# Kernel optimization log

Measured on AMD Instinct MI355X. Metric: run time of the kernel, lower is better.

Reference implementation:

```python
import jax, jax.numpy as jnp
import numpy as np

N_NODES = 100000
N_EDGES = 1600000
D_IN, D_H, D_OUT = 512, 128, 64
BN_EPS = 1e-5


def setup_inputs() -> dict:
    key = jax.random.key(0)
    ks = jax.random.split(key, 8)
    x = jax.random.normal(ks[0], (N_NODES, D_IN), dtype=jnp.float32)
    # COO sparse normalized adjacency
    row = jnp.sort(jax.random.randint(ks[1], (N_EDGES,), 0, N_NODES))
    col = jax.random.randint(ks[2], (N_EDGES,), 0, N_NODES)
    adj_vals = jax.random.uniform(ks[3], (N_EDGES,), dtype=jnp.float32) / 16.0
    # GraphConvolution params (xavier_uniform weight, zero bias)
    lim0 = float(np.sqrt(6.0 / (D_IN + D_H)))
    lim1 = float(np.sqrt(6.0 / (D_H + D_OUT)))
    W0 = jax.random.uniform(ks[4], (D_IN, D_H), minval=-lim0, maxval=lim0, dtype=jnp.float32)
    W1 = jax.random.uniform(ks[5], (D_H, D_OUT), minval=-lim1, maxval=lim1, dtype=jnp.float32)
    b0 = jnp.zeros((D_H,), dtype=jnp.float32)
    b1 = jnp.zeros((D_OUT,), dtype=jnp.float32)
    return {"x": x, "W0": W0, "b0": b0, "W1": W1, "b1": b1,
            "adj_vals": adj_vals, "row": row, "col": col}


def _spmm(vals, row, col, h, n):
    # (sparse adj) @ h : gather source rows, scale by edge value, scatter-add to dest
    return jax.ops.segment_sum(vals[:, None] * h[col], row, num_segments=n)


def reference(x, W0, b0, W1, b1, adj_vals, row, col):
    n = x.shape[0]
    # layer 0: adj @ (x @ W0) + b0  (dropout is identity in eval mode)
    h = _spmm(adj_vals, row, col, x @ W0, n) + b0
    h = jax.nn.relu(h)
    # BatchNorm1d(affine=False, track_running_stats=False): batch stats, biased var
    mean = jnp.mean(h, axis=0)
    var = jnp.mean(jnp.square(h - mean), axis=0)
    h = (h - mean) * jax.lax.rsqrt(var + BN_EPS)
    # layer 1: adj @ (h @ W1) + b1
    return _spmm(adj_vals, row, col, h @ W1, n) + b1
```

## Files before the change

kernel.cpp:

```cpp
#include <hip/hip_runtime.h>
#include <cstdint>
#include <cstddef>

#define D_IN  512
#define D_H   128
#define D_OUT 64

typedef __attribute__((ext_vector_type(8))) short bf16x8;
typedef __attribute__((ext_vector_type(4))) float f32x4;

__device__ __forceinline__ float bf2f(unsigned short u) {
  union { unsigned int i; float f; } v; v.i = ((unsigned int)u) << 16; return v.f;
}
__device__ __forceinline__ unsigned short f2bf(float f) {
  union { unsigned int i; float f; } v; v.f = f;
  unsigned int r = v.i + 0x7FFFu + ((v.i >> 16) & 1u);
  return (unsigned short)(r >> 16);
}

#define OFF_RP    0u
#define OFF_W0T   400384u
#define OFF_W1TP  531456u
#define OFF_SACC  547840u
#define OFF_CVEC  549888u
#define OFF_H     550912u
#define END_H     26150912u
#define END_HW    38950912u

__global__ void k_init(const int* __restrict__ row, int* __restrict__ rp,
                       const float* __restrict__ W0, unsigned short* __restrict__ W0t,
                       float* __restrict__ sacc, int n, int e, int RB, int TB) {
  int b = blockIdx.x, t = threadIdx.x;
  if (b < RB) {
    int i = b * 256 + t;
    if (i > n) return;
    int lo = 0, hi = e;
    while (lo < hi) { int mid = (lo + hi) >> 1; if (row[mid] < i) lo = mid + 1; else hi = mid; }
    rp[i] = lo;
  } else if (b < RB + TB) {
    int idx = (b - RB) * 256 + t;
    int k = idx & (D_IN - 1);
    int nn = idx >> 9;
    W0t[nn * D_IN + k] = f2bf(W0[k * D_H + nn]);
  } else {
    sacc[t] = 0.f;
  }
}

__global__ __launch_bounds__(256) void k_gemm1(const float* __restrict__ A,
                                               const unsigned short* __restrict__ Bt,
                                               unsigned short* __restrict__ C,
                                               int M) {
  __shared__ unsigned short Ash[2][4 * 128 * 8];
  __shared__ unsigned short Bsh[2][4 * 128 * 8];
  const int tid  = threadIdx.x;
  const int lane = tid & 63;
  const int wave = tid >> 6;
  const int wm = (wave >> 1) * 64;
  const int wn = (wave & 1) * 64;
  const int m0 = blockIdx.x * 128;
  const int quad = lane >> 4;
  const int l16  = lane & 15;
  f32x4 acc[4][4] = {};

  int am[2], ak[2];
  const float* aptr[2];
  const unsigned short* bptr[2];
#pragma unroll
  for (int i = 0; i < 2; ++i) {
    int c = tid + i * 256;
    am[i] = c >> 2; ak[i] = c & 3;
    int gm = m0 + am[i]; if (gm >= M) gm = M - 1;
    aptr[i] = A  + (size_t)gm * D_IN + ak[i] * 8;
    bptr[i] = Bt + (size_t)am[i] * D_IN + ak[i] * 8;
  }

  f32x4 areg[2][2];
  bf16x8 breg[2];
#pragma unroll
  for (int i = 0; i < 2; ++i) {
    areg[i][0] = *(const f32x4*)(aptr[i]);
    areg[i][1] = *(const f32x4*)(aptr[i] + 4);
    breg[i]    = *(const bf16x8*)(bptr[i]);
  }

  const int NIT = D_IN / 32;
  for (int it = 0; it < NIT; ++it) {
    const int buf = it & 1;
    unsigned short* ash = Ash[buf];
    unsigned short* bsh = Bsh[buf];
#pragma unroll
    for (int i = 0; i < 2; ++i) {
      bf16x8 pk;
#pragma unroll
      for (int j = 0; j < 4; ++j) {
        pk[j]     = (short)f2bf(areg[i][0][j]);
        pk[4 + j] = (short)f2bf(areg[i][1][j]);
      }
      *(bf16x8*)&ash[(ak[i] * 128 + am[i]) * 8] = pk;
      *(bf16x8*)&bsh[(ak[i] * 128 + am[i]) * 8] = breg[i];
    }
    __syncthreads();
    if (it + 1 < NIT) {
      int k0 = (it + 1) * 32;
#pragma unroll
      for (int i = 0; i < 2; ++i) {
        areg[i][0] = *(const f32x4*)(aptr[i] + k0);
        areg[i][1] = *(const f32x4*)(aptr[i] + k0 + 4);
        breg[i]    = *(const bf16x8*)(bptr[i] + k0);
      }
    }
    bf16x8 af[4], bfv[4];
#pragma unroll
    for (int mf = 0; mf < 4; ++mf)
      af[mf] = *(const bf16x8*)&ash[(quad * 128 + (wm + mf * 16 + l16)) * 8];
#pragma unroll
    for (int nf = 0; nf < 4; ++nf)
      bfv[nf] = *(const bf16x8*)&bsh[(quad * 128 + (wn + nf * 16 + l16)) * 8];
#pragma unroll
    for (int mf = 0; mf < 4; ++mf)
#pragma unroll
      for (int nf = 0; nf < 4; ++nf)
        acc[mf][nf] = __builtin_amdgcn_mfma_f32_16x16x32_bf16(af[mf], bfv[nf], acc[mf][nf], 0, 0, 0);
  }
#pragma unroll
  for (int mf = 0; mf < 4; ++mf)
#pragma unroll
    for (int nf = 0; nf < 4; ++nf)
#pragma unroll
      for (int i = 0; i < 4; ++i) {
        int r = m0 + wm + mf * 16 + quad * 4 + i;
        int cc = wn + nf * 16 + l16;
        if (r < M) C[(size_t)r * D_H + cc] = f2bf(acc[mf][nf][i]);
      }
}

__global__ __launch_bounds__(256) void k_spmm1(const unsigned int* __restrict__ xw2,
                                               const float* __restrict__ adj,
                                               const int* __restrict__ col,
                                               const int* __restrict__ rp,
                                               const float* __restrict__ b0,
                                               unsigned int* __restrict__ h2,
                                               int n) {
  int node = blockIdx.x * 4 + (threadIdx.x >> 6);
  if (node >= n) return;
  int l = threadIdx.x & 63;
  int e0 = rp[node], e1 = rp[node + 1];
  float a0 = 0.f, a1 = 0.f;
  for (int e = e0; e < e1; e += 8) {
    int   idx[8]; float w[8];
#pragma unroll
    for (int j = 0; j < 8; ++j) {
      int ee = e + j;
      int ec = ee < e1 ? ee : e0;
      idx[j] = col[ec];
      w[j] = ee < e1 ? adj[ec] : 0.f;
    }
#pragma unroll
    for (int j = 0; j < 8; ++j) {
      unsigned int p = xw2[(size_t)idx[j] * 64 + l];
      a0 += w[j] * bf2f((unsigned short)(p & 0xFFFF));
      a1 += w[j] * bf2f((unsigned short)(p >> 16));
    }
  }
  float r0 = fmaxf(a0 + b0[2 * l], 0.f);
  float r1 = fmaxf(a1 + b0[2 * l + 1], 0.f);
  h2[(size_t)node * 64 + l] = ((unsigned int)f2bf(r1) << 16) | (unsigned int)f2bf(r0);
}

__global__ __launch_bounds__(256) void k_stats(const unsigned int* __restrict__ h2,
                                               float* __restrict__ sacc, int n) {
  __shared__ float sA[256], sB[256], qA[256], qB[256];
  int t = threadIdx.x;
  int f2 = t & 63, rg = t >> 6;
  float s0 = 0.f, s1 = 0.f, q0 = 0.f, q1 = 0.f;
  for (int r = blockIdx.x * 4 + rg; r < n; r += gridDim.x * 4) {
    unsigned int p = h2[(size_t)r * 64 + f2];
    float v0 = bf2f((unsigned short)(p & 0xFFFF));
    float v1 = bf2f((unsigned short)(p >> 16));
    s0 += v0; s1 += v1; q0 += v0 * v0; q1 += v1 * v1;
  }
  sA[t] = s0; sB[t] = s1; qA[t] = q0; qB[t] = q1;
  __syncthreads();
  if (t < 64) {
    float S0 = sA[t] + sA[t + 64] + sA[t + 128] + sA[t + 192];
    float S1 = sB[t] + sB[t + 64] + sB[t + 128] + sB[t + 192];
    float Q0 = qA[t] + qA[t + 64] + qA[t + 128] + qA[t + 192];
    float Q1 = qB[t] + qB[t + 64] + qB[t + 128] + qB[t + 192];
    atomicAdd(&sacc[2 * t],           S0);
    atomicAdd(&sacc[2 * t + 1],       S1);
    atomicAdd(&sacc[128 + 2 * t],     Q0);
    atomicAdd(&sacc[128 + 2 * t + 1], Q1);
  }
}

__global__ void k_prep2(const float* __restrict__ sacc, const float* __restrict__ W1,
                        unsigned short* __restrict__ W1tp, float* __restrict__ cvec,
                        int n) {
  __shared__ float mean_s[128], istd_s[128];
  int t = threadIdx.x;
  if (t < 128) {
    float m = sacc[t] / (float)n;
    float var = sacc[128 + t] / (float)n - m * m;
    if (var < 0.f) var = 0.f;
    mean_s[t] = m;
    istd_s[t] = rsqrtf(var + 1e-5f);
  }
  __syncthreads();
  for (int idx = t; idx < D_OUT * D_H; idx += 256) {
    int nn = idx >> 7, k = idx & 127;
    W1tp[nn * D_H + k] = f2bf(istd_s[k] * W1[k * D_OUT + nn]);
  }
  if (t < D_OUT) {
    float a = 0.f;
    for (int k = 0; k < D_H; ++k) a += mean_s[k] * istd_s[k] * W1[k * D_OUT + t];
    cvec[t] = -a;
  }
}

__global__ __launch_bounds__(256) void k_gemm2(const unsigned short* __restrict__ A,
                                               const unsigned short* __restrict__ Bt,
                                               const float* __restrict__ cvec,
                                               unsigned short* __restrict__ Cout,
                                               int M) {
  __shared__ unsigned short Ash[4 * 128 * 8];
  __shared__ unsigned short Bsh[4 * 64 * 8];
  const int tid  = threadIdx.x;
  const int lane = tid & 63;
  const int wave = tid >> 6;
  const int wm = wave * 32;
  const int m0 = blockIdx.x * 128;
  const int quad = lane >> 4;
  const int l16  = lane & 15;
  f32x4 acc[2][4] = {};

  for (int k0 = 0; k0 < D_H; k0 += 32) {
    __syncthreads();
#pragma unroll
    for (int i = 0; i < 2; ++i) {
      int c = tid + i * 256;
      int m = c >> 2, k8 = c & 3;
      int gm = m0 + m; if (gm >= M) gm = M - 1;
      *(bf16x8*)&Ash[(k8 * 128 + m) * 8] =
          *(const bf16x8*)&A[(size_t)gm * D_H + k0 + k8 * 8];
    }
    {
      int nn = tid >> 2, k8 = tid & 3;
      *(bf16x8*)&Bsh[(k8 * 64 + nn) * 8] =
          *(const bf16x8*)&Bt[(size_t)nn * D_H + k0 + k8 * 8];
    }
    __syncthreads();
    bf16x8 af[2], bfv[4];
#pragma unroll
    for (int mf = 0; mf < 2; ++mf)
      af[mf] = *(const bf16x8*)&Ash[(quad * 128 + (wm + mf * 16 + l16)) * 8];
#pragma unroll
    for (int nf = 0; nf < 4; ++nf)
      bfv[nf] = *(const bf16x8*)&Bsh[(quad * 64 + (nf * 16 + l16)) * 8];
#pragma unroll
    for (int mf = 0; mf < 2; ++mf)
#pragma unroll
      for (int nf = 0; nf < 4; ++nf)
        acc[mf][nf] = __builtin_amdgcn_mfma_f32_16x16x32_bf16(af[mf], bfv[nf], acc[mf][nf], 0, 0, 0);
  }
#pragma unroll
  for (int mf = 0; mf < 2; ++mf)
#pragma unroll
    for (int nf = 0; nf < 4; ++nf)
#pragma unroll
      for (int i = 0; i < 4; ++i) {
        int r = m0 + wm + mf * 16 + quad * 4 + i;
        int cc = nf * 16 + l16;
        if (r < M) Cout[(size_t)r * 64 + cc] = f2bf(acc[mf][nf][i] + cvec[cc]);
      }
}

__global__ __launch_bounds__(256) void k_spmm2(const unsigned int* __restrict__ hw2,
                                               const float* __restrict__ adj,
                                               const int* __restrict__ col,
                                               const int* __restrict__ rp,
                                               const float* __restrict__ b1,
                                               float2* __restrict__ o2,
                                               int n) {
  int node = blockIdx.x * 8 + (threadIdx.x >> 5);
  if (node >= n) return;
  int l = threadIdx.x & 31;
  int e0 = rp[node], e1 = rp[node + 1];
  float a0 = 0.f, a1 = 0.f;
  for (int e = e0; e < e1; e += 8) {
    int   idx[8]; float w[8];
#pragma unroll
    for (int j = 0; j < 8; ++j) {
      int ee = e + j;
      int ec = ee < e1 ? ee : e0;
      idx[j] = col[ec];
      w[j] = ee < e1 ? adj[ec] : 0.f;
    }
#pragma unroll
    for (int j = 0; j < 8; ++j) {
      unsigned int p = hw2[(size_t)idx[j] * 32 + l];
      a0 += w[j] * bf2f((unsigned short)(p & 0xFFFF));
      a1 += w[j] * bf2f((unsigned short)(p >> 16));
    }
  }
  float2 r; r.x = a0 + b1[2 * l]; r.y = a1 + b1[2 * l + 1];
  o2[(size_t)node * 32 + l] = r;
}

extern "C" void kernel_launch(void* const* d_in, const int* in_sizes, int n_in,
                              void* d_out, int out_size, void* d_ws, size_t ws_size,
                              hipStream_t stream) {
  const float* x   = (const float*)d_in[0];
  const float* W0  = (const float*)d_in[1];
  const float* b0  = (const float*)d_in[2];
  const float* W1  = (const float*)d_in[3];
  const float* b1  = (const float*)d_in[4];
  const float* adj = (const float*)d_in[5];
  const int* row = (const int*)d_in[6];
  const int* col = (const int*)d_in[7];
  const int N = in_sizes[0] / D_IN;
  const int E = in_sizes[5];

  char* ws = (char*)d_ws;
  int*            rp   = (int*)(ws + OFF_RP);
  unsigned short* W0t  = (unsigned short*)(ws + OFF_W0T);
  unsigned short* W1tp = (unsigned short*)(ws + OFF_W1TP);
  float*          sacc = (float*)(ws + OFF_SACC);
  float*          cvec = (float*)(ws + OFF_CVEC);
  unsigned short* h    = (unsigned short*)(ws + OFF_H);

  unsigned short* xw = (unsigned short*)d_out;
  const bool hw_in_ws = (ws_size >= (size_t)END_HW);
  unsigned short* hw   = hw_in_ws ? (unsigned short*)(ws + END_H) : (unsigned short*)d_out;
  float*          outd = hw_in_ws ? (float*)d_out                 : (float*)(ws + OFF_H);

  const int RB = (N + 1 + 255) / 256;
  const int TB = (D_IN * D_H) / 256;
  k_init<<<RB + TB + 1, 256, 0, stream>>>(row, rp, W0, W0t, sacc, N, E, RB, TB);

  k_gemm1<<<(N + 127) / 128, 256, 0, stream>>>(x, W0t, xw, N);
  k_spmm1<<<(N + 3) / 4, 256, 0, stream>>>((const unsigned int*)xw, adj, col, rp, b0,
                                           (unsigned int*)h, N);
  k_stats<<<512, 256, 0, stream>>>((const unsigned int*)h, sacc, N);
  k_prep2<<<1, 256, 0, stream>>>(sacc, W1, W1tp, cvec, N);
  k_gemm2<<<(N + 127) / 128, 256, 0, stream>>>(h, W1tp, cvec, hw, N);
  k_spmm2<<<(N + 7) / 8, 256, 0, stream>>>((const unsigned int*)hw, adj, col, rp, b1,
                                           (float2*)outd, N);

  if (!hw_in_ws) {
    hipMemcpyAsync(d_out, outd, (size_t)N * D_OUT * sizeof(float),
                   hipMemcpyDeviceToDevice, stream);
  }
}
```

Before: 489.5 us.

## Use packed bf16 conversion, unroll SpMM edge loops to 16, replace stats atomics

The fp32-to-bf16 packing in gemm1 now uses the HIP intrinsic __float22bfloat162_rn, converting two values at a time instead of a manual per-element rounding loop. Both SpMM kernels gather 16 edges per iteration instead of 8 to raise memory-level parallelism on the random row gathers. The batch-norm statistics kernel writes per-block partial sums to workspace instead of using global atomics, and the single-block prep kernel reduces the 512 partials serially. The last change also makes the result deterministic, at the cost of more work in the single-block prep kernel and more wasted gathers for nodes with few edges.

```diff
diff --git a/kernel.cpp b/kernel.cpp
--- a/kernel.cpp
+++ b/kernel.cpp
@@ -1,10 +1,12 @@
 #include <hip/hip_runtime.h>
+#include <hip/hip_bf16.h>
 #include <cstdint>
 #include <cstddef>
 
 #define D_IN  512
 #define D_H   128
 #define D_OUT 64
+#define SB    512
 
 typedef __attribute__((ext_vector_type(8))) short bf16x8;
 typedef __attribute__((ext_vector_type(4))) float f32x4;
@@ -17,19 +19,25 @@
   unsigned int r = v.i + 0x7FFFu + ((v.i >> 16) & 1u);
   return (unsigned short)(r >> 16);
 }
+__device__ __forceinline__ unsigned int pk_bf16(float a, float b) {
+  union { __hip_bfloat162 h; unsigned int u; } cv;
+  cv.h = __float22bfloat162_rn(make_float2(a, b));
+  return cv.u;
+}
 
 #define OFF_RP    0u
 #define OFF_W0T   400384u
 #define OFF_W1TP  531456u
-#define OFF_SACC  547840u
-#define OFF_CVEC  549888u
-#define OFF_H     550912u
-#define END_H     26150912u
-#define END_HW    38950912u
+#define OFF_CVEC  547840u
+#define OFF_PSUM  548096u
+#define OFF_PSQ   810240u
+#define OFF_H     1072384u
+#define END_H     26672384u
+#define END_HW    39472384u
 
 __global__ void k_init(const int* __restrict__ row, int* __restrict__ rp,
                        const float* __restrict__ W0, unsigned short* __restrict__ W0t,
-                       float* __restrict__ sacc, int n, int e, int RB, int TB) {
+                       int n, int e, int RB) {
   int b = blockIdx.x, t = threadIdx.x;
   if (b < RB) {
     int i = b * 256 + t;
@@ -37,13 +45,11 @@
     int lo = 0, hi = e;
     while (lo < hi) { int mid = (lo + hi) >> 1; if (row[mid] < i) lo = mid + 1; else hi = mid; }
     rp[i] = lo;
-  } else if (b < RB + TB) {
+  } else {
     int idx = (b - RB) * 256 + t;
     int k = idx & (D_IN - 1);
     int nn = idx >> 9;
     W0t[nn * D_IN + k] = f2bf(W0[k * D_H + nn]);
-  } else {
-    sacc[t] = 0.f;
   }
 }
 
@@ -91,13 +97,12 @@
     unsigned short* bsh = Bsh[buf];
 #pragma unroll
     for (int i = 0; i < 2; ++i) {
-      bf16x8 pk;
-#pragma unroll
-      for (int j = 0; j < 4; ++j) {
-        pk[j]     = (short)f2bf(areg[i][0][j]);
-        pk[4 + j] = (short)f2bf(areg[i][1][j]);
-      }
-      *(bf16x8*)&ash[(ak[i] * 128 + am[i]) * 8] = pk;
+      unsigned int pk4[4];
+      pk4[0] = pk_bf16(areg[i][0][0], areg[i][0][1]);
+      pk4[1] = pk_bf16(areg[i][0][2], areg[i][0][3]);
+      pk4[2] = pk_bf16(areg[i][1][0], areg[i][1][1]);
+      pk4[3] = pk_bf16(areg[i][1][2], areg[i][1][3]);
+      *(uint4*)&ash[(ak[i] * 128 + am[i]) * 8] = *(uint4*)pk4;
       *(bf16x8*)&bsh[(ak[i] * 128 + am[i]) * 8] = breg[i];
     }
     __syncthreads();
@@ -147,17 +152,17 @@
   int l = threadIdx.x & 63;
   int e0 = rp[node], e1 = rp[node + 1];
   float a0 = 0.f, a1 = 0.f;
-  for (int e = e0; e < e1; e += 8) {
-    int   idx[8]; float w[8];
-#pragma unroll
-    for (int j = 0; j < 8; ++j) {
+  for (int e = e0; e < e1; e += 16) {
+    int idx[16]; float w[16];
+#pragma unroll
+    for (int j = 0; j < 16; ++j) {
       int ee = e + j;
       int ec = ee < e1 ? ee : e0;
       idx[j] = col[ec];
       w[j] = ee < e1 ? adj[ec] : 0.f;
     }
 #pragma unroll
-    for (int j = 0; j < 8; ++j) {
+    for (int j = 0; j < 16; ++j) {
       unsigned int p = xw2[(size_t)idx[j] * 64 + l];
       a0 += w[j] * bf2f((unsigned short)(p & 0xFFFF));
       a1 += w[j] * bf2f((unsigned short)(p >> 16));
@@ -169,7 +174,8 @@
 }
 
 __global__ __launch_bounds__(256) void k_stats(const unsigned int* __restrict__ h2,
-                                               float* __restrict__ sacc, int n) {
+                                               float* __restrict__ psum,
+                                               float* __restrict__ psq, int n) {
   __shared__ float sA[256], sB[256], qA[256], qB[256];
   int t = threadIdx.x;
   int f2 = t & 63, rg = t >> 6;
@@ -187,21 +193,25 @@
     float S1 = sB[t] + sB[t + 64] + sB[t + 128] + sB[t + 192];
     float Q0 = qA[t] + qA[t + 64] + qA[t + 128] + qA[t + 192];
     float Q1 = qB[t] + qB[t + 64] + qB[t + 128] + qB[t + 192];
-    atomicAdd(&sacc[2 * t],           S0);
-    atomicAdd(&sacc[2 * t + 1],       S1);
-    atomicAdd(&sacc[128 + 2 * t],     Q0);
-    atomicAdd(&sacc[128 + 2 * t + 1], Q1);
-  }
-}
-
-__global__ void k_prep2(const float* __restrict__ sacc, const float* __restrict__ W1,
+    psum[blockIdx.x * 128 + 2 * t]     = S0;
+    psum[blockIdx.x * 128 + 2 * t + 1] = S1;
+    psq [blockIdx.x * 128 + 2 * t]     = Q0;
+    psq [blockIdx.x * 128 + 2 * t + 1] = Q1;
+  }
+}
+
+__global__ void k_prep2(const float* __restrict__ psum, const float* __restrict__ psq,
+                        const float* __restrict__ W1,
                         unsigned short* __restrict__ W1tp, float* __restrict__ cvec,
                         int n) {
   __shared__ float mean_s[128], istd_s[128];
   int t = threadIdx.x;
   if (t < 128) {
-    float m = sacc[t] / (float)n;
-    float var = sacc[128 + t] / (float)n - m * m;
+    float s = 0.f, q = 0.f;
+#pragma unroll 4
+    for (int b = 0; b < SB; ++b) { s += psum[b * 128 + t]; q += psq[b * 128 + t]; }
+    float m = s / (float)n;
+    float var = q / (float)n - m * m;
     if (var < 0.f) var = 0.f;
     mean_s[t] = m;
     istd_s[t] = rsqrtf(var + 1e-5f);
@@ -287,17 +297,17 @@
   int l = threadIdx.x & 31;
   int e0 = rp[node], e1 = rp[node + 1];
   float a0 = 0.f, a1 = 0.f;
-  for (int e = e0; e < e1; e += 8) {
-    int   idx[8]; float w[8];
-#pragma unroll
-    for (int j = 0; j < 8; ++j) {
+  for (int e = e0; e < e1; e += 16) {
+    int idx[16]; float w[16];
+#pragma unroll
+    for (int j = 0; j < 16; ++j) {
       int ee = e + j;
       int ec = ee < e1 ? ee : e0;
       idx[j] = col[ec];
       w[j] = ee < e1 ? adj[ec] : 0.f;
     }
 #pragma unroll
-    for (int j = 0; j < 8; ++j) {
+    for (int j = 0; j < 16; ++j) {
       unsigned int p = hw2[(size_t)idx[j] * 32 + l];
       a0 += w[j] * bf2f((unsigned short)(p & 0xFFFF));
       a1 += w[j] * bf2f((unsigned short)(p >> 16));
@@ -325,8 +335,9 @@
   int*            rp   = (int*)(ws + OFF_RP);
   unsigned short* W0t  = (unsigned short*)(ws + OFF_W0T);
   unsigned short* W1tp = (unsigned short*)(ws + OFF_W1TP);
-  float*          sacc = (float*)(ws + OFF_SACC);
   float*          cvec = (float*)(ws + OFF_CVEC);
+  float*          psum = (float*)(ws + OFF_PSUM);
+  float*          psq  = (float*)(ws + OFF_PSQ);
   unsigned short* h    = (unsigned short*)(ws + OFF_H);
 
   unsigned short* xw = (unsigned short*)d_out;
@@ -336,13 +347,13 @@
 
   const int RB = (N + 1 + 255) / 256;
   const int TB = (D_IN * D_H) / 256;
-  k_init<<<RB + TB + 1, 256, 0, stream>>>(row, rp, W0, W0t, sacc, N, E, RB, TB);
+  k_init<<<RB + TB, 256, 0, stream>>>(row, rp, W0, W0t, N, E, RB);
 
   k_gemm1<<<(N + 127) / 128, 256, 0, stream>>>(x, W0t, xw, N);
   k_spmm1<<<(N + 3) / 4, 256, 0, stream>>>((const unsigned int*)xw, adj, col, rp, b0,
                                            (unsigned int*)h, N);
-  k_stats<<<512, 256, 0, stream>>>((const unsigned int*)h, sacc, N);
-  k_prep2<<<1, 256, 0, stream>>>(sacc, W1, W1tp, cvec, N);
+  k_stats<<<SB, 256, 0, stream>>>((const unsigned int*)h, psum, psq, N);
+  k_prep2<<<1, 256, 0, stream>>>(psum, psq, W1, W1tp, cvec, N);
   k_gemm2<<<(N + 127) / 128, 256, 0, stream>>>(h, W1tp, cvec, hw, N);
   k_spmm2<<<(N + 7) / 8, 256, 0, stream>>>((const unsigned int*)hw, adj, col, rp, b1,
                                            (float2*)outd, N);
```

After: 515.5 us. 5.3% more time.
